# Optimization experiments

Measured on AMD Instinct MI355X. Metric: run time of the kernel, lower is better.

Reference implementation:

```python
import jax, jax.numpy as jnp
import numpy as np

N_NODES = 100000


def _gcn_conv(x, src, dst, dinv, W, b, n):
    # x: [n, din] -> [n, dout]; PyG GCNConv: transform, then normalized scatter-sum, then bias
    h = x @ W                                   # [n, dout]
    norm = dinv[src] * dinv[dst]                # [E'] symmetric normalization
    msg = h[src] * norm[:, None]                # gather + scale (irregular access)
    out = jax.ops.segment_sum(msg, dst, num_segments=n)
    return out + b


def _add_self_loops(edge_index, n):
    loop = jnp.arange(n, dtype=edge_index.dtype)
    src = jnp.concatenate([edge_index[0], loop])
    dst = jnp.concatenate([edge_index[1], loop])
    return src, dst


def setup_inputs() -> dict:
    key = jax.random.key(0)
    k1, k2, k3, k4 = jax.random.split(key, 4)
    n, e = N_NODES, 1000000
    din, dhid, dout = 512, 512, 128
    x = jax.random.normal(k1, (n, din), dtype=jnp.float32)
    edge_index = jax.random.randint(k2, (2, e), 0, n, dtype=jnp.int64)
    W1 = jax.random.normal(k3, (din, dhid), dtype=jnp.float32) * (1.0 / np.sqrt(din))
    b1 = jnp.zeros((dhid,), dtype=jnp.float32)
    W2 = jax.random.normal(k4, (dhid, dout), dtype=jnp.float32) * (1.0 / np.sqrt(dhid))
    b2 = jnp.zeros((dout,), dtype=jnp.float32)
    return {"x": x, "edge_index": edge_index, "original_size": n,
            "W1": W1, "b1": b1, "W2": W2, "b2": b2}


def reference(x, edge_index, original_size, W1, b1, W2, b2):
    n = x.shape[0]
    src, dst = _add_self_loops(edge_index, n)
    # degree over destination (with self-loops deg >= 1)
    deg = jnp.zeros((n,), dtype=x.dtype).at[dst].add(1.0)
    dinv = deg ** -0.5
    h = _gcn_conv(x, src, dst, dinv, W1, b1, n)
    out = _gcn_conv(h, src, dst, dinv, W2, b2, n)
    return out[:original_size]
```

## Files before the change

kernel.cpp:

```cpp
#include <hip/hip_runtime.h>
#include <hip/hip_bf16.h>


typedef __attribute__((ext_vector_type(8))) short short8;
typedef __attribute__((ext_vector_type(4))) float f32x4;

#define DIN 512
#define DOUT 128

__device__ inline short f2bs(float f) {
    __hip_bfloat16 h = __float2bfloat16(f);
    return __builtin_bit_cast(short, h);
}
__device__ inline float b2f(const void* p, long long idx) {
    return __bfloat162float(((const __hip_bfloat16*)p)[idx]);
}
__device__ inline int edge_at(const void* ei, int eflag, long long idx) {
    return eflag ? ((const int*)ei)[idx] : (int)((const long long*)ei)[idx];
}

__global__ void k_fdetect(const unsigned short* __restrict__ xr, int* __restrict__ fflag) {
    __shared__ int cnt;
    if (threadIdx.x == 0) cnt = 0;
    __syncthreads();
    int local = 0;
    for (int i = threadIdx.x; i < 8192; i += 256) {
        unsigned e = (xr[i] >> 7) & 0xFF;
        if (e == 0 || (e >= 0x70 && e <= 0x8E)) local++;
    }
    atomicAdd(&cnt, local);
    __syncthreads();
    if (threadIdx.x == 0) *fflag = (cnt >= 7373) ? 1 : 0;
}

__global__ void k_edetect(const int* __restrict__ ei_raw, int* __restrict__ eflag) {
    __shared__ int any;
    if (threadIdx.x == 0) any = 0;
    __syncthreads();
    for (int i = threadIdx.x; i < 4096; i += 256)
        if (ei_raw[2 * i + 1] != 0) any = 1;
    __syncthreads();
    if (threadIdx.x == 0) *eflag = any;
}

__global__ __launch_bounds__(256) void k_w12(const void* __restrict__ W1,
                                             const void* __restrict__ W2,
                                             const int* __restrict__ fflag,
                                             __hip_bfloat16* __restrict__ w12t) {
    int t = blockIdx.x * 256 + threadIdx.x;
    int d = t >> 7, j = t & 127;
    float acc = 0.f;
    if (*fflag) {
        for (int c = 0; c < 512; ++c)
            acc += b2f(W1, d * 512 + c) * b2f(W2, c * 128 + j);
    } else {
        const float* w1 = (const float*)W1;
        const float* w2 = (const float*)W2;
        for (int c = 0; c < 512; ++c)
            acc += w1[d * 512 + c] * w2[c * 128 + j];
    }
    w12t[j * 512 + d] = __float2bfloat16(acc);
}

__global__ void k_b12(const void* __restrict__ b1, const void* __restrict__ W2,
                      const int* __restrict__ fflag, float* __restrict__ b12) {
    int j = threadIdx.x;
    float acc = 0.f;
    if (*fflag) {
        for (int c = 0; c < 512; ++c)
            acc += b2f(b1, c) * b2f(W2, c * 128 + j);
    } else {
        const float* bb = (const float*)b1;
        const float* w2 = (const float*)W2;
        for (int c = 0; c < 512; ++c)
            acc += bb[c] * w2[c * 128 + j];
    }
    b12[j] = acc;
}

__global__ __launch_bounds__(256) void k_deg(const void* __restrict__ ei,
                                             const int* __restrict__ eflag, int E,
                                             int* __restrict__ degi) {
    int e = blockIdx.x * 256 + threadIdx.x;
    if (e >= E) return;
    atomicAdd(&degi[edge_at(ei, *eflag, (long long)E + e)], 1);
}

__global__ __launch_bounds__(256) void k_dinv(const int* __restrict__ degi,
                                              float* __restrict__ dinv, int n) {
    int i = blockIdx.x * 256 + threadIdx.x;
    if (i >= n) return;
    dinv[i] = rsqrtf((float)(degi[i] + 1));
}

__global__ __launch_bounds__(256) void k_scan1(const int* __restrict__ degi,
                                               int* __restrict__ row_ptr,
                                               int* __restrict__ blocksum, int n) {
    __shared__ int sh[256];
    int t = threadIdx.x, g = blockIdx.x * 256 + t;
    int val = (g < n) ? degi[g] : 0;
    sh[t] = val;
    __syncthreads();
    for (int o = 1; o < 256; o <<= 1) {
        int v = (t >= o) ? sh[t - o] : 0;
        __syncthreads();
        if (t >= o) sh[t] += v;
        __syncthreads();
    }
    if (g < n) row_ptr[g] = sh[t] - val;
    if (t == 255) blocksum[blockIdx.x] = sh[255];
}

__global__ void k_scan2(int* __restrict__ blocksum, int nb) {
    __shared__ int sh[512];
    int t = threadIdx.x;
    int val = (t < nb) ? blocksum[t] : 0;
    sh[t] = val;
    __syncthreads();
    for (int o = 1; o < 512; o <<= 1) {
        int v = (t >= o) ? sh[t - o] : 0;
        __syncthreads();
        if (t >= o) sh[t] += v;
        __syncthreads();
    }
    if (t < nb) blocksum[t] = sh[t] - val;
}

__global__ __launch_bounds__(256) void k_scan3(int* __restrict__ row_ptr,
                                               int* __restrict__ cursor,
                                               const int* __restrict__ blocksum,
                                               int n, int E) {
    int g = blockIdx.x * 256 + threadIdx.x;
    if (g == 0) row_ptr[n] = E;
    if (g >= n) return;
    int v = row_ptr[g] + blocksum[blockIdx.x];
    row_ptr[g] = v;
    cursor[g] = v;
}

__global__ __launch_bounds__(256) void k_fill(const void* __restrict__ ei,
                                              const int* __restrict__ eflag, int E,
                                              const float* __restrict__ dinv,
                                              int* __restrict__ cursor,
                                              int2* __restrict__ csr) {
    int e = blockIdx.x * 256 + threadIdx.x;
    if (e >= E) return;
    int f = *eflag;
    int s = edge_at(ei, f, e);
    int d = edge_at(ei, f, (long long)E + e);
    int pos = atomicAdd(&cursor[d], 1);
    csr[pos] = make_int2(s, __float_as_int(dinv[s]));
}

__global__ __launch_bounds__(256) void k_gemm(const void* __restrict__ xv,
                                              const __hip_bfloat16* __restrict__ w12t,
                                              const int* __restrict__ fflag,
                                              float* __restrict__ M, int n) {
    int wave = (blockIdx.x * 256 + threadIdx.x) >> 6;
    int lane = threadIdx.x & 63;
    int row0 = wave * 32;
    if (row0 >= n) return;
    int quad = lane >> 4, m16 = lane & 15;
    const short* ws = (const short*)w12t;

    f32x4 acc[2][8];
#pragma unroll
    for (int i = 0; i < 2; ++i)
#pragma unroll
        for (int j = 0; j < 8; ++j) acc[i][j] = (f32x4){0.f, 0.f, 0.f, 0.f};

    int ra = row0 + m16, rb = row0 + 16 + m16;
    if (ra >= n) ra = n - 1;
    if (rb >= n) rb = n - 1;

    if (*fflag) {
        const short* xs = (const short*)xv;
#pragma unroll 2
        for (int ks = 0; ks < 16; ++ks) {
            int k0 = ks * 32 + quad * 8;
            short8 A0 = *(const short8*)(xs + (size_t)ra * 512 + k0);
            short8 A1 = *(const short8*)(xs + (size_t)rb * 512 + k0);
#pragma unroll
            for (int nc = 0; nc < 8; ++nc) {
                short8 B = *(const short8*)(ws + (nc * 16 + m16) * 512 + k0);
                acc[0][nc] = __builtin_amdgcn_mfma_f32_16x16x32_bf16(A0, B, acc[0][nc], 0, 0, 0);
                acc[1][nc] = __builtin_amdgcn_mfma_f32_16x16x32_bf16(A1, B, acc[1][nc], 0, 0, 0);
            }
        }
    } else {
        const float* xf = (const float*)xv;
#pragma unroll 2
        for (int ks = 0; ks < 16; ++ks) {
            int k0 = ks * 32 + quad * 8;
            float4 u0 = *(const float4*)(xf + (size_t)ra * 512 + k0);
            float4 u1 = *(const float4*)(xf + (size_t)ra * 512 + k0 + 4);
            float4 v0 = *(const float4*)(xf + (size_t)rb * 512 + k0);
            float4 v1 = *(const float4*)(xf + (size_t)rb * 512 + k0 + 4);
            short8 A0, A1;
            A0[0] = f2bs(u0.x); A0[1] = f2bs(u0.y); A0[2] = f2bs(u0.z); A0[3] = f2bs(u0.w);
            A0[4] = f2bs(u1.x); A0[5] = f2bs(u1.y); A0[6] = f2bs(u1.z); A0[7] = f2bs(u1.w);
            A1[0] = f2bs(v0.x); A1[1] = f2bs(v0.y); A1[2] = f2bs(v0.z); A1[3] = f2bs(v0.w);
            A1[4] = f2bs(v1.x); A1[5] = f2bs(v1.y); A1[6] = f2bs(v1.z); A1[7] = f2bs(v1.w);
#pragma unroll
            for (int nc = 0; nc < 8; ++nc) {
                short8 B = *(const short8*)(ws + (nc * 16 + m16) * 512 + k0);
                acc[0][nc] = __builtin_amdgcn_mfma_f32_16x16x32_bf16(A0, B, acc[0][nc], 0, 0, 0);
                acc[1][nc] = __builtin_amdgcn_mfma_f32_16x16x32_bf16(A1, B, acc[1][nc], 0, 0, 0);
            }
        }
    }
#pragma unroll
    for (int rt = 0; rt < 2; ++rt)
#pragma unroll
        for (int nc = 0; nc < 8; ++nc)
#pragma unroll
            for (int r = 0; r < 4; ++r) {
                int row = row0 + rt * 16 + quad * 4 + r;
                if (row < n)
                    M[(size_t)row * 128 + nc * 16 + m16] = acc[rt][nc][r];
            }
}

template <bool FINAL>
__global__ __launch_bounds__(256) void k_gather(const int* __restrict__ row_ptr,
                                                const int2* __restrict__ csr,
                                                const float* __restrict__ dinv,
                                                const float* __restrict__ src_feat,
                                                float* __restrict__ dstf,
                                                const float* __restrict__ b12,
                                                const void* __restrict__ b2,
                                                const int* __restrict__ fflag,
                                                void* __restrict__ out, int n) {
    int d = blockIdx.x * 4 + (threadIdx.x >> 6);
    if (d >= n) return;
    int lane = threadIdx.x & 63;
    int c = lane * 2;
    float di = dinv[d];
    float2 self = *(const float2*)(src_feat + (size_t)d * 128 + c);
    float ax = di * self.x, ay = di * self.y;
    float wsum = 0.f;
    int beg = row_ptr[d], end = row_ptr[d + 1];
    for (int e = beg; e < end; ++e) {
        int2 rec = csr[e];
        float w = __int_as_float(rec.y);
        float2 v = *(const float2*)(src_feat + (size_t)rec.x * 128 + c);
        ax += w * v.x;
        ay += w * v.y;
        wsum += w;
    }
    ax *= di;
    ay *= di;
    if (!FINAL) {
        *(float2*)(dstf + (size_t)d * 128 + c) = make_float2(ax, ay);
    } else {
        float coef = di * (wsum + di);
        if (*fflag) {
            unsigned short o0 = (unsigned short)f2bs(ax + coef * b12[c]     + b2f(b2, c));
            unsigned short o1 = (unsigned short)f2bs(ay + coef * b12[c + 1] + b2f(b2, c + 1));
            *(ushort2*)((unsigned short*)out + (size_t)d * 128 + c) = make_ushort2(o0, o1);
        } else {
            float o0 = ax + coef * b12[c]     + ((const float*)b2)[c];
            float o1 = ay + coef * b12[c + 1] + ((const float*)b2)[c + 1];
            *(float2*)((float*)out + (size_t)d * 128 + c) = make_float2(o0, o1);
        }
    }
}

__global__ __launch_bounds__(256) void k_sentinel(unsigned short* __restrict__ out, int total) {
    int t = blockIdx.x * 256 + threadIdx.x;
    if (t < total) out[t] = 0x4641;
}

extern "C" void kernel_launch(void* const* d_in, const int* in_sizes, int n_in,
                              void* d_out, int out_size, void* d_ws, size_t ws_size,
                              hipStream_t stream) {
    const int n = out_size / DOUT;

    const void *x = nullptr, *W1 = nullptr, *b1 = nullptr, *W2 = nullptr, *b2 = nullptr;
    const void* ei_raw = nullptr;
    int E = 0;
    const long long nx = (long long)n * DIN;
    for (int i = 0; i < n_in; ++i) {
        long long s = in_sizes[i];
        if      (s == nx && !x)                      x  = d_in[i];
        else if (s == (long long)DIN * DIN && !W1)   W1 = d_in[i];
        else if (s == (long long)DIN && !b1)         b1 = d_in[i];
        else if (s == (long long)DIN * DOUT && !W2)  W2 = d_in[i];
        else if (s == (long long)DOUT && !b2)        b2 = d_in[i];
        else if (s == 1) {  }
        else if (!ei_raw) { ei_raw = d_in[i]; E = (int)(s / 2); }
    }
    if (!x || !W1 || !b1 || !W2 || !b2 || !ei_raw) {
        x  = d_in[0];
        ei_raw = d_in[1];  E = in_sizes[1] / 2;
        W1 = d_in[3]; b1 = d_in[4]; W2 = d_in[5]; b2 = d_in[6];
    }

    const int nb_scan = (n + 255) / 256;

    char* ws = (char*)d_ws;
    size_t off = 0;
    auto alloc = [&](size_t bytes) { void* p = ws + off; off = (off + bytes + 255) & ~255ULL; return p; };
    int*   eflag    = (int*)alloc(4);
    int*   fflag    = (int*)alloc(4);
    int*   degi     = (int*)alloc((size_t)n * 4);
    float* dinv     = (float*)alloc((size_t)n * 4);
    float* b12      = (float*)alloc(DOUT * 4);
    __hip_bfloat16* w12t = (__hip_bfloat16*)alloc(DIN * DOUT * 2);
    int*   row_ptr  = (int*)alloc(((size_t)n + 1) * 4);
    int*   cursor   = (int*)alloc((size_t)n * 4);
    int*   blocksum = (int*)alloc(512 * 4);
    int2*  csr      = (int2*)alloc((size_t)E * 8);
    float* M        = (float*)alloc((size_t)n * DOUT * 4);
    float* B1       = (float*)alloc((size_t)n * DOUT * 4);

    if (ws_size < off) {
        k_sentinel<<<(out_size + 255) / 256, 256, 0, stream>>>((unsigned short*)d_out, out_size);
        return;
    }

    hipMemsetAsync(degi, 0, (size_t)n * 4, stream);

    k_fdetect<<<1, 256, 0, stream>>>((const unsigned short*)x, fflag);
    k_edetect<<<1, 256, 0, stream>>>((const int*)ei_raw, eflag);

    k_w12<<<(DIN * DOUT) / 256, 256, 0, stream>>>(W1, W2, fflag, w12t);
    k_b12<<<1, 128, 0, stream>>>(b1, W2, fflag, b12);

    k_deg<<<(E + 255) / 256, 256, 0, stream>>>(ei_raw, eflag, E, degi);
    k_dinv<<<(n + 255) / 256, 256, 0, stream>>>(degi, dinv, n);
    k_scan1<<<nb_scan, 256, 0, stream>>>(degi, row_ptr, blocksum, n);
    k_scan2<<<1, 512, 0, stream>>>(blocksum, nb_scan);
    k_scan3<<<nb_scan, 256, 0, stream>>>(row_ptr, cursor, blocksum, n, E);
    k_fill<<<(E + 255) / 256, 256, 0, stream>>>(ei_raw, eflag, E, dinv, cursor, csr);

    int waves = (n + 31) / 32;
    k_gemm<<<(waves + 3) / 4, 256, 0, stream>>>(x, w12t, fflag, M, n);

    int nb_g = (n + 3) / 4;
    k_gather<false><<<nb_g, 256, 0, stream>>>(row_ptr, csr, dinv, M, B1,
                                              nullptr, nullptr, fflag, nullptr, n);
    k_gather<true><<<nb_g, 256, 0, stream>>>(row_ptr, csr, dinv, B1, nullptr,
                                             b12, b2, fflag, d_out, n);
}
```

Before: 747.5 us.

## Prepack fused weight for MFMA, shrink GEMM tile, split-edge float4 gather, fuse dinv

Stores the fused W1·W2 weight in an MFMA-fragment-packed layout so each lane loads its B operand with one contiguous, coalesced 16-byte access. The GEMM now handles 16 rows per wave instead of 32, which lowers register pressure and doubles the number of waves, at the cost of reading the B operand twice as often. The gather kernels split each node's edges between two half-waves with float4 loads and combine the halves with a cross-lane shuffle, aiming for more memory-level parallelism. The dinv computation is folded into the first scan kernel, removing one launch.

```diff
diff --git a/kernel.cpp b/kernel.cpp
--- a/kernel.cpp
+++ b/kernel.cpp
@@ -46,7 +46,7 @@
 __global__ __launch_bounds__(256) void k_w12(const void* __restrict__ W1,
                                              const void* __restrict__ W2,
                                              const int* __restrict__ fflag,
-                                             __hip_bfloat16* __restrict__ w12t) {
+                                             __hip_bfloat16* __restrict__ w12p) {
     int t = blockIdx.x * 256 + threadIdx.x;
     int d = t >> 7, j = t & 127;
     float acc = 0.f;
@@ -59,7 +59,10 @@
         for (int c = 0; c < 512; ++c)
             acc += w1[d * 512 + c] * w2[c * 128 + j];
     }
-    w12t[j * 512 + d] = __float2bfloat16(acc);
+    int ks = d >> 5, r = d & 31;
+    int quad = r >> 3, jj = r & 7;
+    int nc = j >> 4, m16 = j & 15;
+    w12p[(((size_t)(ks * 8 + nc) * 64) + quad * 16 + m16) * 8 + jj] = __float2bfloat16(acc);
 }
 
 __global__ void k_b12(const void* __restrict__ b1, const void* __restrict__ W2,
@@ -86,19 +89,14 @@
     atomicAdd(&degi[edge_at(ei, *eflag, (long long)E + e)], 1);
 }
 
-__global__ __launch_bounds__(256) void k_dinv(const int* __restrict__ degi,
-                                              float* __restrict__ dinv, int n) {
-    int i = blockIdx.x * 256 + threadIdx.x;
-    if (i >= n) return;
-    dinv[i] = rsqrtf((float)(degi[i] + 1));
-}
-
 __global__ __launch_bounds__(256) void k_scan1(const int* __restrict__ degi,
                                                int* __restrict__ row_ptr,
-                                               int* __restrict__ blocksum, int n) {
+                                               int* __restrict__ blocksum,
+                                               float* __restrict__ dinv, int n) {
     __shared__ int sh[256];
     int t = threadIdx.x, g = blockIdx.x * 256 + t;
     int val = (g < n) ? degi[g] : 0;
+    if (g < n) dinv[g] = rsqrtf((float)(val + 1));
     sh[t] = val;
     __syncthreads();
     for (int o = 1; o < 256; o <<= 1) {
@@ -153,72 +151,60 @@
 }
 
 __global__ __launch_bounds__(256) void k_gemm(const void* __restrict__ xv,
-                                              const __hip_bfloat16* __restrict__ w12t,
+                                              const short* __restrict__ w12p,
                                               const int* __restrict__ fflag,
                                               float* __restrict__ M, int n) {
     int wave = (blockIdx.x * 256 + threadIdx.x) >> 6;
     int lane = threadIdx.x & 63;
-    int row0 = wave * 32;
+    int row0 = wave * 16;
     if (row0 >= n) return;
     int quad = lane >> 4, m16 = lane & 15;
-    const short* ws = (const short*)w12t;
-
-    f32x4 acc[2][8];
-#pragma unroll
-    for (int i = 0; i < 2; ++i)
-#pragma unroll
-        for (int j = 0; j < 8; ++j) acc[i][j] = (f32x4){0.f, 0.f, 0.f, 0.f};
-
-    int ra = row0 + m16, rb = row0 + 16 + m16;
+    const short8* Bp = (const short8*)w12p;
+
+    f32x4 acc[8];
+#pragma unroll
+    for (int j = 0; j < 8; ++j) acc[j] = (f32x4){0.f, 0.f, 0.f, 0.f};
+
+    int ra = row0 + m16;
     if (ra >= n) ra = n - 1;
-    if (rb >= n) rb = n - 1;
 
     if (*fflag) {
         const short* xs = (const short*)xv;
-#pragma unroll 2
+#pragma unroll 4
         for (int ks = 0; ks < 16; ++ks) {
             int k0 = ks * 32 + quad * 8;
             short8 A0 = *(const short8*)(xs + (size_t)ra * 512 + k0);
-            short8 A1 = *(const short8*)(xs + (size_t)rb * 512 + k0);
 #pragma unroll
             for (int nc = 0; nc < 8; ++nc) {
-                short8 B = *(const short8*)(ws + (nc * 16 + m16) * 512 + k0);
-                acc[0][nc] = __builtin_amdgcn_mfma_f32_16x16x32_bf16(A0, B, acc[0][nc], 0, 0, 0);
-                acc[1][nc] = __builtin_amdgcn_mfma_f32_16x16x32_bf16(A1, B, acc[1][nc], 0, 0, 0);
+                short8 B = Bp[(ks * 8 + nc) * 64 + lane];
+                acc[nc] = __builtin_amdgcn_mfma_f32_16x16x32_bf16(A0, B, acc[nc], 0, 0, 0);
             }
         }
     } else {
         const float* xf = (const float*)xv;
-#pragma unroll 2
+#pragma unroll 4
         for (int ks = 0; ks < 16; ++ks) {
             int k0 = ks * 32 + quad * 8;
             float4 u0 = *(const float4*)(xf + (size_t)ra * 512 + k0);
             float4 u1 = *(const float4*)(xf + (size_t)ra * 512 + k0 + 4);
-            float4 v0 = *(const float4*)(xf + (size_t)rb * 512 + k0);
-            float4 v1 = *(const float4*)(xf + (size_t)rb * 512 + k0 + 4);
-            short8 A0, A1;
+            short8 A0;
             A0[0] = f2bs(u0.x); A0[1] = f2bs(u0.y); A0[2] = f2bs(u0.z); A0[3] = f2bs(u0.w);
             A0[4] = f2bs(u1.x); A0[5] = f2bs(u1.y); A0[6] = f2bs(u1.z); A0[7] = f2bs(u1.w);
-            A1[0] = f2bs(v0.x); A1[1] = f2bs(v0.y); A1[2] = f2bs(v0.z); A1[3] = f2bs(v0.w);
-            A1[4] = f2bs(v1.x); A1[5] = f2bs(v1.y); A1[6] = f2bs(v1.z); A1[7] = f2bs(v1.w);
 #pragma unroll
             for (int nc = 0; nc < 8; ++nc) {
-                short8 B = *(const short8*)(ws + (nc * 16 + m16) * 512 + k0);
-                acc[0][nc] = __builtin_amdgcn_mfma_f32_16x16x32_bf16(A0, B, acc[0][nc], 0, 0, 0);
-                acc[1][nc] = __builtin_amdgcn_mfma_f32_16x16x32_bf16(A1, B, acc[1][nc], 0, 0, 0);
+                short8 B = Bp[(ks * 8 + nc) * 64 + lane];
+                acc[nc] = __builtin_amdgcn_mfma_f32_16x16x32_bf16(A0, B, acc[nc], 0, 0, 0);
             }
         }
     }
 #pragma unroll
-    for (int rt = 0; rt < 2; ++rt)
-#pragma unroll
-        for (int nc = 0; nc < 8; ++nc)
-#pragma unroll
-            for (int r = 0; r < 4; ++r) {
-                int row = row0 + rt * 16 + quad * 4 + r;
-                if (row < n)
-                    M[(size_t)row * 128 + nc * 16 + m16] = acc[rt][nc][r];
-            }
+    for (int nc = 0; nc < 8; ++nc)
+#pragma unroll
+        for (int r = 0; r < 4; ++r) {
+            int row = row0 + quad * 4 + r;
+            if (row < n)
+                M[(size_t)row * 128 + nc * 16 + m16] = acc[nc][r];
+        }
 }
 
 template <bool FINAL>
@@ -234,34 +220,49 @@
     int d = blockIdx.x * 4 + (threadIdx.x >> 6);
     if (d >= n) return;
     int lane = threadIdx.x & 63;
-    int c = lane * 2;
+    int half = lane >> 5, sl = lane & 31;
+    int c = sl * 4;
     float di = dinv[d];
-    float2 self = *(const float2*)(src_feat + (size_t)d * 128 + c);
-    float ax = di * self.x, ay = di * self.y;
-    float wsum = 0.f;
+    float ax = 0.f, ay = 0.f, az = 0.f, aw = 0.f, wsum = 0.f;
+    if (half == 0) {
+        float4 s = *(const float4*)(src_feat + (size_t)d * 128 + c);
+        ax = di * s.x; ay = di * s.y; az = di * s.z; aw = di * s.w;
+    }
     int beg = row_ptr[d], end = row_ptr[d + 1];
-    for (int e = beg; e < end; ++e) {
+    for (int e = beg + half; e < end; e += 2) {
         int2 rec = csr[e];
         float w = __int_as_float(rec.y);
-        float2 v = *(const float2*)(src_feat + (size_t)rec.x * 128 + c);
-        ax += w * v.x;
-        ay += w * v.y;
+        float4 v = *(const float4*)(src_feat + (size_t)rec.x * 128 + c);
+        ax += w * v.x; ay += w * v.y; az += w * v.z; aw += w * v.w;
         wsum += w;
     }
-    ax *= di;
-    ay *= di;
+    ax += __shfl_xor(ax, 32);
+    ay += __shfl_xor(ay, 32);
+    az += __shfl_xor(az, 32);
+    aw += __shfl_xor(aw, 32);
+    wsum += __shfl_xor(wsum, 32);
+    if (half) return;
+    ax *= di; ay *= di; az *= di; aw *= di;
     if (!FINAL) {
-        *(float2*)(dstf + (size_t)d * 128 + c) = make_float2(ax, ay);
+        *(float4*)(dstf + (size_t)d * 128 + c) = make_float4(ax, ay, az, aw);
     } else {
         float coef = di * (wsum + di);
+        float o0 = ax + coef * b12[c];
+        float o1 = ay + coef * b12[c + 1];
+        float o2 = az + coef * b12[c + 2];
+        float o3 = aw + coef * b12[c + 3];
         if (*fflag) {
-            unsigned short o0 = (unsigned short)f2bs(ax + coef * b12[c]     + b2f(b2, c));
-            unsigned short o1 = (unsigned short)f2bs(ay + coef * b12[c + 1] + b2f(b2, c + 1));
-            *(ushort2*)((unsigned short*)out + (size_t)d * 128 + c) = make_ushort2(o0, o1);
+            o0 += b2f(b2, c);     o1 += b2f(b2, c + 1);
+            o2 += b2f(b2, c + 2); o3 += b2f(b2, c + 3);
+            ushort4 u = make_ushort4((unsigned short)f2bs(o0), (unsigned short)f2bs(o1),
+                                     (unsigned short)f2bs(o2), (unsigned short)f2bs(o3));
+            *(ushort4*)((unsigned short*)out + (size_t)d * 128 + c) = u;
         } else {
-            float o0 = ax + coef * b12[c]     + ((const float*)b2)[c];
-            float o1 = ay + coef * b12[c + 1] + ((const float*)b2)[c + 1];
-            *(float2*)((float*)out + (size_t)d * 128 + c) = make_float2(o0, o1);
+            o0 += ((const float*)b2)[c];
+            o1 += ((const float*)b2)[c + 1];
+            o2 += ((const float*)b2)[c + 2];
+            o3 += ((const float*)b2)[c + 3];
+            *(float4*)((float*)out + (size_t)d * 128 + c) = make_float4(o0, o1, o2, o3);
         }
     }
 }
@@ -306,7 +307,7 @@
     int*   degi     = (int*)alloc((size_t)n * 4);
     float* dinv     = (float*)alloc((size_t)n * 4);
     float* b12      = (float*)alloc(DOUT * 4);
-    __hip_bfloat16* w12t = (__hip_bfloat16*)alloc(DIN * DOUT * 2);
+    __hip_bfloat16* w12p = (__hip_bfloat16*)alloc(DIN * DOUT * 2);
     int*   row_ptr  = (int*)alloc(((size_t)n + 1) * 4);
     int*   cursor   = (int*)alloc((size_t)n * 4);
     int*   blocksum = (int*)alloc(512 * 4);
@@ -324,18 +325,17 @@
     k_fdetect<<<1, 256, 0, stream>>>((const unsigned short*)x, fflag);
     k_edetect<<<1, 256, 0, stream>>>((const int*)ei_raw, eflag);
 
-    k_w12<<<(DIN * DOUT) / 256, 256, 0, stream>>>(W1, W2, fflag, w12t);
+    k_w12<<<(DIN * DOUT) / 256, 256, 0, stream>>>(W1, W2, fflag, w12p);
     k_b12<<<1, 128, 0, stream>>>(b1, W2, fflag, b12);
 
     k_deg<<<(E + 255) / 256, 256, 0, stream>>>(ei_raw, eflag, E, degi);
-    k_dinv<<<(n + 255) / 256, 256, 0, stream>>>(degi, dinv, n);
-    k_scan1<<<nb_scan, 256, 0, stream>>>(degi, row_ptr, blocksum, n);
+    k_scan1<<<nb_scan, 256, 0, stream>>>(degi, row_ptr, blocksum, dinv, n);
     k_scan2<<<1, 512, 0, stream>>>(blocksum, nb_scan);
     k_scan3<<<nb_scan, 256, 0, stream>>>(row_ptr, cursor, blocksum, n, E);
     k_fill<<<(E + 255) / 256, 256, 0, stream>>>(ei_raw, eflag, E, dinv, cursor, csr);
 
-    int waves = (n + 31) / 32;
-    k_gemm<<<(waves + 3) / 4, 256, 0, stream>>>(x, w12t, fflag, M, n);
+    int waves = (n + 15) / 16;
+    k_gemm<<<(waves + 3) / 4, 256, 0, stream>>>(x, (const short*)w12p, fflag, M, n);
 
     int nb_g = (n + 3) / 4;
     k_gather<false><<<nb_g, 256, 0, stream>>>(row_ptr, csr, dinv, M, B1,
```

Result: faster. 697.2 us (-6.7%).
